# Optimization experiments

Measured on AMD Instinct MI355X. Metric: run time of the kernel, lower is better.

## Reference

```python
import jax, jax.numpy as jnp
import numpy as np

V, E, H, K, B, T = 32000, 512, 1024, 64, 64, 512


def setup_inputs() -> dict:
    key = jax.random.key(0)
    ks = jax.random.split(key, 12)
    nrm = lambda k, shape, sc: jax.random.normal(k, shape, jnp.float32) * sc
    inv_sqrt_h = 1.0 / np.sqrt(H)
    return {
        "x": jax.random.randint(ks[0], (B, T), 0, V),
        "tags": jax.random.randint(ks[1], (B, T), 0, K),
        "emb": nrm(ks[2], (V, E), 0.02),
        "w_ih": nrm(ks[3], (3 * H, E), inv_sqrt_h),
        "w_hh": nrm(ks[4], (3 * H, H), inv_sqrt_h),
        "b_ih": nrm(ks[5], (3 * H,), 0.01),
        "b_hh": nrm(ks[6], (3 * H,), 0.01),
        "fc_w": nrm(ks[7], (K, H), inv_sqrt_h),
        "fc_b": jnp.zeros((K,), jnp.float32),
        "start_trans": nrm(ks[8], (K,), 0.1),
        "end_trans": nrm(ks[9], (K,), 0.1),
        "trans": nrm(ks[10], (K, K), 0.1),
    }


def gru_scan(x_seq, w_ih, w_hh, b_ih, b_hh):
    # x_seq: [T, B, E] -> hidden states [T, B, H]; torch nn.GRU equations.
    Bn = x_seq.shape[1]
    Hd = w_hh.shape[1]
    # precompute input projections for all steps: [T, B, 3H]
    gi = jnp.einsum('tbe,ge->tbg', x_seq, w_ih) + b_ih

    def step(h, gi_t):
        gh = h @ w_hh.T + b_hh                      # [B, 3H]
        i_r, i_z, i_n = jnp.split(gi_t, 3, axis=-1)
        h_r, h_z, h_n = jnp.split(gh, 3, axis=-1)
        r = jax.nn.sigmoid(i_r + h_r)
        z = jax.nn.sigmoid(i_z + h_z)
        n = jnp.tanh(i_n + r * h_n)
        h_new = (1.0 - z) * n + z * h
        return h_new, h_new

    h0 = jnp.zeros((Bn, Hd), x_seq.dtype)
    _, hs = jax.lax.scan(step, h0, gi)
    return hs


def crf_nll(emissions, tags, start, end, trans):
    # emissions [B, T, K], tags [B, T]; torchcrf CRF, mask=None, reduction='sum'.
    em_t = jnp.swapaxes(emissions, 0, 1)   # [T, B, K]
    tg_t = jnp.swapaxes(tags, 0, 1)        # [T, B]
    Bn = emissions.shape[0]
    bidx = jnp.arange(Bn)

    # numerator: score of the gold path
    num0 = start[tg_t[0]] + em_t[0, bidx, tg_t[0]]

    def num_step(acc, xs):
        em_i, tag_prev, tag_cur = xs
        acc = acc + trans[tag_prev, tag_cur] + em_i[bidx, tag_cur]
        return acc, None

    num, _ = jax.lax.scan(num_step, num0, (em_t[1:], tg_t[:-1], tg_t[1:]))
    num = num + end[tg_t[-1]]

    # denominator: forward algorithm (log partition)
    alpha0 = start + em_t[0]                # [B, K]

    def den_step(alpha, em_i):
        # alpha[b,i] + trans[i,j] + em_i[b,j] -> logsumexp over i
        nxt = jax.scipy.special.logsumexp(
            alpha[:, :, None] + trans[None, :, :] + em_i[:, None, :], axis=1)
        return nxt, None

    alpha, _ = jax.lax.scan(den_step, alpha0, em_t[1:])
    den = jax.scipy.special.logsumexp(alpha + end, axis=1)
    return jnp.sum(den - num)  # = -sum(log-likelihood) = model's returned loss


def reference(x, tags, emb, w_ih, w_hh, b_ih, b_hh, fc_w, fc_b,
              start_trans, end_trans, trans):
    xe = emb[x]                              # [B, T, E]
    hs = gru_scan(jnp.swapaxes(xe, 0, 1), w_ih, w_hh, b_ih, b_hh)  # [T, B, H]
    gru_out = jnp.swapaxes(hs, 0, 1)         # [B, T, H]
    emissions = gru_out @ fc_w.T + fc_b      # [B, T, K]
    return crf_nll(emissions, tags, start_trans, end_trans, trans)
```

## Files before the change

### kernel.cpp

```cpp
#include <hip/hip_runtime.h>

typedef unsigned short USH;
typedef unsigned int u32;
typedef unsigned long long u64;
typedef float v4f __attribute__((ext_vector_type(4)));
typedef __bf16 v8bf __attribute__((ext_vector_type(8)));
typedef u32 v4u __attribute__((ext_vector_type(4)));

#define B_ 64
#define T_ 512
#define E_ 512
#define H_ 1024
#define NSCAN 128

__device__ __forceinline__ USH f2b(float x) {
  union { float f; u32 u; } v; v.f = x;
  u32 r = v.u + 0x7FFFu + ((v.u >> 16) & 1u);
  return (USH)(r >> 16);
}
__device__ __forceinline__ v8bf ldb8(const USH* p) {
  uint4 u = *reinterpret_cast<const uint4*>(p);
  return __builtin_bit_cast(v8bf, u);
}
__device__ __forceinline__ v4f MF(v8bf a, v8bf b, v4f c) {
  return __builtin_amdgcn_mfma_f32_16x16x32_bf16(a, b, c, 0, 0, 0);
}
__device__ __forceinline__ float sigm(float x) { return 1.0f / (1.0f + __expf(-x)); }
__device__ __forceinline__ float tanhx(float x) { return 1.0f - 2.0f / (__expf(2.0f * x) + 1.0f); }

__device__ __forceinline__ v4u ldc16(u64 a) {
  v4u d;
  asm volatile("global_load_dwordx4 %0, %1, off sc0 sc1" : "=v"(d) : "v"(a));
  return d;
}
__device__ __forceinline__ void stc16(u64 a, v4u d) {
  asm volatile("global_store_dwordx4 %0, %1, off sc1" :: "v"(a), "v"(d) : "memory");
}

__global__ void castk(const float* __restrict__ s, USH* __restrict__ d, int n) {
  int i = (blockIdx.x * 256 + threadIdx.x) * 4;
  if (i >= n) return;
  float4 v = *reinterpret_cast<const float4*>(s + i);
  ushort4 q = make_ushort4(f2b(v.x), f2b(v.y), f2b(v.z), f2b(v.w));
  *reinterpret_cast<ushort4*>(d + i) = q;
}

__global__ void gatherk(const int* __restrict__ x, const float* __restrict__ emb, USH* __restrict__ xeb) {
  int r = blockIdx.x;
  int id = x[r];
  const float4* e = reinterpret_cast<const float4*>(emb + (long)id * E_);
  float4 v = e[threadIdx.x];
  ushort4 q = make_ushort4(f2b(v.x), f2b(v.y), f2b(v.z), f2b(v.w));
  *reinterpret_cast<ushort4*>(xeb + (long)r * E_ + threadIdx.x * 4) = q;
}

__global__ __launch_bounds__(256, 1) void fused(
    const USH* __restrict__ xeb, const USH* __restrict__ wihB, const USH* __restrict__ whhB,
    const float* __restrict__ bih, const float* __restrict__ bhh, char* __restrict__ hsC,
    const USH* __restrict__ fcwB, const float* __restrict__ fcb, float* __restrict__ em)
{
  __shared__ float redS[6144];
  __shared__ USH  trpS[512];

  const int tid = threadIdx.x;
  const int wv = tid >> 6, ln = tid & 63;
  const int l16 = ln & 15, lq = ln >> 4;
  const v4f z4 = {0.f, 0.f, 0.f, 0.f};

  if (blockIdx.x < NSCAN) {
    const int bg = blockIdx.x >> 6, cb = blockIdx.x & 63;
    const int b0 = bg * 32, c0 = cb * 16;

    v8bf wihf[4][3], whhf[8][3];
    #pragma unroll
    for (int kt = 0; kt < 4; ++kt)
      #pragma unroll
      for (int g = 0; g < 3; ++g)
        wihf[kt][g] = ldb8(wihB + (size_t)(g * H_ + c0 + l16) * E_ + (wv * 16 + kt * 4 + lq) * 8);
    #pragma unroll
    for (int kt = 0; kt < 8; ++kt)
      #pragma unroll
      for (int g = 0; g < 3; ++g)
        whhf[kt][g] = ldb8(whhB + (size_t)(g * H_ + c0 + l16) * H_ + (wv * 32 + kt * 4 + lq) * 8);

    const int cgl = c0 + l16;
    const float bir = bih[cgl], biz = bih[H_ + cgl], bin = bih[2 * H_ + cgl];
    const float bhr = bhh[cgl], bhz = bhh[H_ + cgl], bhn = bhh[2 * H_ + cgl];

    const USH* a1b = xeb + (size_t)(b0 + l16) * (T_ * E_) + wv * 128 + 8 * lq;
    const u64 hC = (u64)(uintptr_t)hsC + (u64)bg * 65536;
    const int lane_off = (wv * 16 + (lq >> 1)) * 1024 + l16 * 32 + (lq & 1) * 16;
    const u64 probe_off = (u64)((wv * 16 + l16) * 1024 + 1020);

    float hp0 = 0.f, hp1 = 0.f, hp2 = 0.f, hp3 = 0.f;
    v4f* rv = reinterpret_cast<v4f*>(redS);

    uint4 pf[8];
    #pragma unroll
    for (int kt = 0; kt < 4; ++kt) {
      pf[kt * 2]     = *reinterpret_cast<const uint4*>(a1b + kt * 32);
      pf[kt * 2 + 1] = *reinterpret_cast<const uint4*>(a1b + 16 * (T_ * E_) + kt * 32);
    }
    u32 pr = 0;

    for (int t = 0; t < T_; ++t) {
      v4f acc[8];
      #pragma unroll
      for (int i = 0; i < 8; ++i) acc[i] = z4;

      #pragma unroll
      for (int kt = 0; kt < 4; ++kt) {
        v8bf a0 = __builtin_bit_cast(v8bf, pf[kt * 2]);
        v8bf a1f = __builtin_bit_cast(v8bf, pf[kt * 2 + 1]);
        acc[0] = MF(a0, wihf[kt][0], acc[0]); acc[1] = MF(a1f, wihf[kt][0], acc[1]);
        acc[2] = MF(a0, wihf[kt][1], acc[2]); acc[3] = MF(a1f, wihf[kt][1], acc[3]);
        acc[4] = MF(a0, wihf[kt][2], acc[4]); acc[5] = MF(a1f, wihf[kt][2], acc[5]);
      }

      if (t > 0) {
        const u64 hbase = hC + (u64)(t - 1) * 131072;
        while (true) {
          asm volatile("s_waitcnt vmcnt(0)" ::: "memory");
          __builtin_amdgcn_sched_barrier(0);
          if (__ballot(pr != 0xFFFFFFFFu) == ~0ull) break;
          asm volatile("global_load_dword %0, %1, off sc0 sc1" : "=v"(pr) : "v"(hbase + probe_off));
        }
        v4u ha[16];
        while (true) {
          #pragma unroll
          for (int kt = 0; kt < 8; ++kt) {
            ha[kt * 2]     = ldc16(hbase + lane_off + kt * 2048);
            ha[kt * 2 + 1] = ldc16(hbase + lane_off + kt * 2048 + 512);
          }
          asm volatile("s_waitcnt vmcnt(0)" ::: "memory");
          __builtin_amdgcn_sched_barrier(0);
          bool bad = false;
          #pragma unroll
          for (int f = 0; f < 16; ++f) {
            #pragma unroll
            for (int d = 0; d < 4; ++d) bad |= (ha[f][d] == 0xFFFFFFFFu);
          }
          if (__ballot(bad) == 0ull) break;
        }
        #pragma unroll
        for (int kt = 0; kt < 8; ++kt) {
          v8bf a0 = __builtin_bit_cast(v8bf, ha[kt * 2]);
          v8bf a1f = __builtin_bit_cast(v8bf, ha[kt * 2 + 1]);
          acc[0] = MF(a0, whhf[kt][0], acc[0]); acc[1] = MF(a1f, whhf[kt][0], acc[1]);
          acc[2] = MF(a0, whhf[kt][1], acc[2]); acc[3] = MF(a1f, whhf[kt][1], acc[3]);
          acc[6] = MF(a0, whhf[kt][2], acc[6]); acc[7] = MF(a1f, whhf[kt][2], acc[7]);
        }
      }

      if (wv >= 2) {
        #pragma unroll
        for (int f = 0; f < 8; ++f) rv[(wv - 2) * 512 + f * 64 + ln] = acc[f];
      } else if (wv == 0) {
        #pragma unroll
        for (int j = 0; j < 4; ++j) rv[1024 + j * 64 + ln] = acc[2 * j + 1];
      } else {
        #pragma unroll
        for (int j = 0; j < 4; ++j) rv[1280 + j * 64 + ln] = acc[2 * j];
      }
      __syncthreads();

      if (wv < 2) {
        v4f m0, m1, m2, m3;
        if (wv == 0) {
          m0 = acc[0]; m1 = acc[2]; m2 = acc[4]; m3 = acc[6];
          #pragma unroll
          for (int w = 0; w < 2; ++w) {
            m0 += rv[w * 512 + 0 * 64 + ln]; m1 += rv[w * 512 + 2 * 64 + ln];
            m2 += rv[w * 512 + 4 * 64 + ln]; m3 += rv[w * 512 + 6 * 64 + ln];
          }
          m0 += rv[1280 + 0 * 64 + ln]; m1 += rv[1280 + 1 * 64 + ln];
          m2 += rv[1280 + 2 * 64 + ln]; m3 += rv[1280 + 3 * 64 + ln];
        } else {
          m0 = acc[1]; m1 = acc[3]; m2 = acc[5]; m3 = acc[7];
          #pragma unroll
          for (int w = 0; w < 2; ++w) {
            m0 += rv[w * 512 + 1 * 64 + ln]; m1 += rv[w * 512 + 3 * 64 + ln];
            m2 += rv[w * 512 + 5 * 64 + ln]; m3 += rv[w * 512 + 7 * 64 + ln];
          }
          m0 += rv[1024 + 0 * 64 + ln]; m1 += rv[1024 + 1 * 64 + ln];
          m2 += rv[1024 + 2 * 64 + ln]; m3 += rv[1024 + 3 * 64 + ln];
        }
        #pragma unroll
        for (int r4 = 0; r4 < 4; ++r4) {
          float rg = sigm(m0[r4] + bir + bhr);
          float zg = sigm(m1[r4] + biz + bhz);
          float ng = tanhx(m2[r4] + bin + rg * (m3[r4] + bhn));
          float hprev = (r4 == 0 ? hp0 : r4 == 1 ? hp1 : r4 == 2 ? hp2 : hp3);
          float hn = (1.f - zg) * ng + zg * hprev;
          if (r4 == 0) hp0 = hn; else if (r4 == 1) hp1 = hn; else if (r4 == 2) hp2 = hn; else hp3 = hn;
          trpS[(wv * 16 + lq * 4 + r4) * 16 + l16] = f2b(hn);
        }
        if (ln < 32) {
          v4u hv = *reinterpret_cast<const v4u*>(trpS + wv * 256 + ln * 8);
          stc16(hC + (u64)t * 131072 + (u64)cb * 1024 + (u64)(wv * 512) + (u64)ln * 16, hv);
        }
      }

      {
        const u64 hb = hC + (u64)t * 131072;
        asm volatile("global_load_dword %0, %1, off sc0 sc1" : "=v"(pr) : "v"(hb + probe_off));
        const USH* a1n = a1b + (size_t)(t + 1 < T_ ? t + 1 : t) * E_;
        #pragma unroll
        for (int kt = 0; kt < 4; ++kt) {
          pf[kt * 2]     = *reinterpret_cast<const uint4*>(a1n + kt * 32);
          pf[kt * 2 + 1] = *reinterpret_cast<const uint4*>(a1n + 16 * (T_ * E_) + kt * 32);
        }
      }
    }
  } else {
    const int e = blockIdx.x - NSCAN;
    v8bf fcf[8][4];
    #pragma unroll
    for (int kt = 0; kt < 8; ++kt)
      #pragma unroll
      for (int nt = 0; nt < 4; ++nt)
        fcf[kt][nt] = ldb8(fcwB + (size_t)(nt * 16 + l16) * H_ + wv * 256 + kt * 32 + 8 * lq);
    float bias[4];
    #pragma unroll
    for (int nt = 0; nt < 4; ++nt) bias[nt] = fcb[nt * 16 + l16];

    v4f* rvE = reinterpret_cast<v4f*>(redS);
    for (int i = 0; i < 16; ++i) {
      int tile = i * 128 + e, t = tile >> 2, bq = tile & 3;
      const u64 ab = (u64)(uintptr_t)hsC + (u64)t * 131072 + (u64)(bq >> 1) * 65536
                   + (u64)((bq & 1) * 16 + l16) * 32 + (u64)(wv * 16 + (lq >> 1)) * 1024 + (u64)(lq & 1) * 16;
      v4u ha[8];
      while (true) {
        #pragma unroll
        for (int kt = 0; kt < 8; ++kt) ha[kt] = ldc16(ab + kt * 2048);
        asm volatile("s_waitcnt vmcnt(0)" ::: "memory");
        __builtin_amdgcn_sched_barrier(0);
        bool bad = false;
        #pragma unroll
        for (int kt = 0; kt < 8; ++kt) {
          #pragma unroll
          for (int d = 0; d < 4; ++d) bad |= (ha[kt][d] == 0xFFFFFFFFu);
        }
        if (__ballot(bad) == 0ull) break;
        __builtin_amdgcn_s_sleep(32);
      }
      v4f acc[4];
      #pragma unroll
      for (int nt = 0; nt < 4; ++nt) acc[nt] = z4;
      #pragma unroll
      for (int kt = 0; kt < 8; ++kt) {
        v8bf a = __builtin_bit_cast(v8bf, ha[kt]);
        #pragma unroll
        for (int nt = 0; nt < 4; ++nt) acc[nt] = MF(a, fcf[kt][nt], acc[nt]);
      }
      __syncthreads();
      if (wv != 0) {
        #pragma unroll
        for (int nt = 0; nt < 4; ++nt) rvE[(wv - 1) * 256 + nt * 64 + ln] = acc[nt];
      }
      __syncthreads();
      if (wv == 0) {
        #pragma unroll
        for (int nt = 0; nt < 4; ++nt) {
          v4f s = acc[nt];
          #pragma unroll
          for (int w = 0; w < 3; ++w) s += rvE[w * 256 + nt * 64 + ln];
          int k = nt * 16 + l16;
          #pragma unroll
          for (int r = 0; r < 4; ++r) {
            int b = bq * 16 + lq * 4 + r;
            em[((size_t)b * T_ + t) * 64 + k] = s[r] + bias[nt];
          }
        }
      }
    }
  }
}

__global__ __launch_bounds__(64) void crfk(const float* __restrict__ em, const int* __restrict__ tags,
                                           const float* __restrict__ st, const float* __restrict__ en,
                                           const float* __restrict__ tr, float* __restrict__ res) {
  int b = blockIdx.x, j = threadIdx.x;
  __shared__ float trs[4096];
  for (int i = j; i < 4096; i += 64) trs[i] = tr[i];
  __syncthreads();
  const int* tg = tags + b * T_;
  const float* e = em + (long)b * T_ * 64;
  float np = 0.f;
  for (int t = j; t < T_; t += 64) {
    int ct = tg[t];
    np += e[t * 64 + ct];
    if (t > 0) np += trs[tg[t - 1] * 64 + ct];
  }
  #pragma unroll
  for (int o = 32; o; o >>= 1) np += __shfl_xor(np, o, 64);
  float num = np + st[tg[0]] + en[tg[T_ - 1]];
  float alpha = st[j] + e[j];
  for (int t = 1; t < T_; ++t) {
    float vv[64];
    #pragma unroll
    for (int i = 0; i < 64; ++i) vv[i] = __shfl(alpha, i, 64) + trs[i * 64 + j];
    float mc[4];
    #pragma unroll
    for (int c = 0; c < 4; ++c) {
      mc[c] = vv[c * 16];
      #pragma unroll
      for (int ii = 1; ii < 16; ++ii) mc[c] = fmaxf(mc[c], vv[c * 16 + ii]);
    }
    float M = fmaxf(fmaxf(mc[0], mc[1]), fmaxf(mc[2], mc[3]));
    float sc[4] = {0.f, 0.f, 0.f, 0.f};
    #pragma unroll
    for (int c = 0; c < 4; ++c)
      #pragma unroll
      for (int ii = 0; ii < 16; ++ii) sc[c] += __expf(vv[c * 16 + ii] - M);
    alpha = M + __logf((sc[0] + sc[1]) + (sc[2] + sc[3])) + e[t * 64 + j];
  }
  float v = alpha + en[j];
  float mm = v;
  #pragma unroll
  for (int o = 32; o; o >>= 1) mm = fmaxf(mm, __shfl_xor(mm, o, 64));
  float ss = __expf(v - mm);
  #pragma unroll
  for (int o = 32; o; o >>= 1) ss += __shfl_xor(ss, o, 64);
  if (j == 0) res[b] = (mm + __logf(ss)) - num;
}

__global__ void fin(const float* __restrict__ res, float* __restrict__ out) {
  float v = res[threadIdx.x];
  #pragma unroll
  for (int o = 32; o; o >>= 1) v += __shfl_xor(v, o, 64);
  if (threadIdx.x == 0) out[0] = v;
}

extern "C" void kernel_launch(void* const* d_in, const int* in_sizes, int n_in,
                              void* d_out, int out_size, void* d_ws, size_t ws_size,
                              hipStream_t stream) {
  (void)in_sizes; (void)n_in; (void)out_size;
  const int*   x    = (const int*)d_in[0];
  const int*   tags = (const int*)d_in[1];
  const float* emb  = (const float*)d_in[2];
  const float* wih  = (const float*)d_in[3];
  const float* whh  = (const float*)d_in[4];
  const float* bih  = (const float*)d_in[5];
  const float* bhh  = (const float*)d_in[6];
  const float* fcw  = (const float*)d_in[7];
  const float* fcb  = (const float*)d_in[8];
  const float* str  = (const float*)d_in[9];
  const float* enr  = (const float*)d_in[10];
  const float* trn  = (const float*)d_in[11];

  char* ws = (char*)d_ws;
  USH*   xeb  = (USH*)(ws + 0);
  USH*   wihB = (USH*)(ws + 33554432);
  USH*   whhB = (USH*)(ws + 36700160);
  USH*   fcwB = (USH*)(ws + 42991616);
  char*  hsC  = (char*)(ws + 43122688);
  float* em   = (float*)(ws + 110231552);
  float* res  = (float*)(ws + 118620160);
  if (ws_size < 118620416ull) return;

  hipMemsetAsync(hsC, 0xFF, 67108864, stream);

  castk<<<1536, 256, 0, stream>>>(wih, wihB, 3 * H_ * E_);
  castk<<<3072, 256, 0, stream>>>(whh, whhB, 3 * H_ * H_);
  castk<<<64, 256, 0, stream>>>(fcw, fcwB, 64 * H_);
  gatherk<<<B_ * T_, 128, 0, stream>>>(x, emb, xeb);
  fused<<<256, 256, 0, stream>>>(xeb, wihB, whhB, bih, bhh, hsC, fcwB, fcb, em);
  crfk<<<B_, 64, 0, stream>>>(em, tags, str, enr, trn, res);
  fin<<<1, 64, 0, stream>>>(res, (float*)d_out);
}
```

Baseline: 2.685 ms.

## Fuse weight casts, CRF and final reduction into persistent kernel with flag sync

Removes the separate bf16 cast kernels by converting the fp32 weights to bf16 inside the fused kernel as they are loaded into registers. The CRF forward pass and the final sum become extra blocks of the persistent kernel that poll emission and result sentinels, so they overlap with the GRU scan. The scan's cross-block wait now uses per-column-block step-counter flags and speculatively prefetches the next hidden state, falling back to flag polling only when sentinels remain. This cuts launches and the serial CRF tail, but adds more spin-polling traffic and a smaller emission block count.

```diff
diff --git a/kernel.cpp b/kernel.cpp
--- a/kernel.cpp
+++ b/kernel.cpp
@@ -12,15 +12,21 @@
 #define E_ 512
 #define H_ 1024
 #define NSCAN 128
+#define EMIT0 128
+#define NEMIT 111
+#define CRF0  239
+#define FINB  255
 
 __device__ __forceinline__ USH f2b(float x) {
   union { float f; u32 u; } v; v.f = x;
   u32 r = v.u + 0x7FFFu + ((v.u >> 16) & 1u);
   return (USH)(r >> 16);
 }
-__device__ __forceinline__ v8bf ldb8(const USH* p) {
-  uint4 u = *reinterpret_cast<const uint4*>(p);
-  return __builtin_bit_cast(v8bf, u);
+__device__ __forceinline__ v8bf pack8(float4 a, float4 b) {
+  union { USH s[8]; v8bf v; } r;
+  r.s[0] = f2b(a.x); r.s[1] = f2b(a.y); r.s[2] = f2b(a.z); r.s[3] = f2b(a.w);
+  r.s[4] = f2b(b.x); r.s[5] = f2b(b.y); r.s[6] = f2b(b.z); r.s[7] = f2b(b.w);
+  return r.v;
 }
 __device__ __forceinline__ v4f MF(v8bf a, v8bf b, v4f c) {
   return __builtin_amdgcn_mfma_f32_16x16x32_bf16(a, b, c, 0, 0, 0);
@@ -36,13 +42,8 @@
 __device__ __forceinline__ void stc16(u64 a, v4u d) {
   asm volatile("global_store_dwordx4 %0, %1, off sc1" :: "v"(a), "v"(d) : "memory");
 }
-
-__global__ void castk(const float* __restrict__ s, USH* __restrict__ d, int n) {
-  int i = (blockIdx.x * 256 + threadIdx.x) * 4;
-  if (i >= n) return;
-  float4 v = *reinterpret_cast<const float4*>(s + i);
-  ushort4 q = make_ushort4(f2b(v.x), f2b(v.y), f2b(v.z), f2b(v.w));
-  *reinterpret_cast<ushort4*>(d + i) = q;
+__device__ __forceinline__ void stdw(u64 a, u32 v) {
+  asm volatile("global_store_dword %0, %1, off sc1" :: "v"(a), "v"(v) : "memory");
 }
 
 __global__ void gatherk(const int* __restrict__ x, const float* __restrict__ emb, USH* __restrict__ xeb) {
@@ -55,9 +56,12 @@
 }
 
 __global__ __launch_bounds__(256, 1) void fused(
-    const USH* __restrict__ xeb, const USH* __restrict__ wihB, const USH* __restrict__ whhB,
+    const USH* __restrict__ xeb, const float* __restrict__ wih, const float* __restrict__ whh,
     const float* __restrict__ bih, const float* __restrict__ bhh, char* __restrict__ hsC,
-    const USH* __restrict__ fcwB, const float* __restrict__ fcb, float* __restrict__ em)
+    u32* __restrict__ flags, const float* __restrict__ fcw, const float* __restrict__ fcb,
+    float* __restrict__ em, const int* __restrict__ tags, const float* __restrict__ stv,
+    const float* __restrict__ env, const float* __restrict__ trn, float* __restrict__ res,
+    float* __restrict__ outp)
 {
   __shared__ float redS[6144];
   __shared__ USH  trpS[512];
@@ -75,13 +79,19 @@
     #pragma unroll
     for (int kt = 0; kt < 4; ++kt)
       #pragma unroll
-      for (int g = 0; g < 3; ++g)
-        wihf[kt][g] = ldb8(wihB + (size_t)(g * H_ + c0 + l16) * E_ + (wv * 16 + kt * 4 + lq) * 8);
+      for (int g = 0; g < 3; ++g) {
+        const float* wp = wih + (size_t)(g * H_ + c0 + l16) * E_ + (wv * 16 + kt * 4 + lq) * 8;
+        wihf[kt][g] = pack8(*reinterpret_cast<const float4*>(wp),
+                            *reinterpret_cast<const float4*>(wp + 4));
+      }
     #pragma unroll
     for (int kt = 0; kt < 8; ++kt)
       #pragma unroll
-      for (int g = 0; g < 3; ++g)
-        whhf[kt][g] = ldb8(whhB + (size_t)(g * H_ + c0 + l16) * H_ + (wv * 32 + kt * 4 + lq) * 8);
+      for (int g = 0; g < 3; ++g) {
+        const float* wp = whh + (size_t)(g * H_ + c0 + l16) * H_ + (wv * 32 + kt * 4 + lq) * 8;
+        whhf[kt][g] = pack8(*reinterpret_cast<const float4*>(wp),
+                            *reinterpret_cast<const float4*>(wp + 4));
+      }
 
     const int cgl = c0 + l16;
     const float bir = bih[cgl], biz = bih[H_ + cgl], bin = bih[2 * H_ + cgl];
@@ -90,7 +100,8 @@
     const USH* a1b = xeb + (size_t)(b0 + l16) * (T_ * E_) + wv * 128 + 8 * lq;
     const u64 hC = (u64)(uintptr_t)hsC + (u64)bg * 65536;
     const int lane_off = (wv * 16 + (lq >> 1)) * 1024 + l16 * 32 + (lq & 1) * 16;
-    const u64 probe_off = (u64)((wv * 16 + l16) * 1024 + 1020);
+    const u64 flv = (u64)(uintptr_t)(flags + (bg * 64 + wv * 16 + l16));
+    const u64 myfl = (u64)(uintptr_t)(flags + (bg * 64 + cb));
 
     float hp0 = 0.f, hp1 = 0.f, hp2 = 0.f, hp3 = 0.f;
     v4f* rv = reinterpret_cast<v4f*>(redS);
@@ -101,7 +112,8 @@
       pf[kt * 2]     = *reinterpret_cast<const uint4*>(a1b + kt * 32);
       pf[kt * 2 + 1] = *reinterpret_cast<const uint4*>(a1b + 16 * (T_ * E_) + kt * 32);
     }
-    u32 pr = 0;
+    u32 fr = 0;
+    v4u ha[16];
 
     for (int t = 0; t < T_; ++t) {
       v4f acc[8];
@@ -119,28 +131,37 @@
 
       if (t > 0) {
         const u64 hbase = hC + (u64)(t - 1) * 131072;
-        while (true) {
-          asm volatile("s_waitcnt vmcnt(0)" ::: "memory");
-          __builtin_amdgcn_sched_barrier(0);
-          if (__ballot(pr != 0xFFFFFFFFu) == ~0ull) break;
-          asm volatile("global_load_dword %0, %1, off sc0 sc1" : "=v"(pr) : "v"(hbase + probe_off));
-        }
-        v4u ha[16];
-        while (true) {
-          #pragma unroll
-          for (int kt = 0; kt < 8; ++kt) {
-            ha[kt * 2]     = ldc16(hbase + lane_off + kt * 2048);
-            ha[kt * 2 + 1] = ldc16(hbase + lane_off + kt * 2048 + 512);
+        asm volatile("s_waitcnt vmcnt(0)" ::: "memory");
+        __builtin_amdgcn_sched_barrier(0);
+        bool bad = false;
+        #pragma unroll
+        for (int f = 0; f < 16; ++f) {
+          #pragma unroll
+          for (int d = 0; d < 4; ++d) bad |= (ha[f][d] == 0xFFFFFFFFu);
+        }
+        if (__ballot(bad) != 0ull) {
+          while (__ballot(fr >= (u32)t) != ~0ull) {
+            asm volatile("global_load_dword %0, %1, off sc0 sc1" : "=v"(fr) : "v"(flv));
+            asm volatile("s_waitcnt vmcnt(0)" ::: "memory");
+            __builtin_amdgcn_sched_barrier(0);
           }
-          asm volatile("s_waitcnt vmcnt(0)" ::: "memory");
-          __builtin_amdgcn_sched_barrier(0);
-          bool bad = false;
-          #pragma unroll
-          for (int f = 0; f < 16; ++f) {
+          while (true) {
             #pragma unroll
-            for (int d = 0; d < 4; ++d) bad |= (ha[f][d] == 0xFFFFFFFFu);
+            for (int kt = 0; kt < 8; ++kt) {
+              ha[kt * 2]     = ldc16(hbase + lane_off + kt * 2048);
+              ha[kt * 2 + 1] = ldc16(hbase + lane_off + kt * 2048 + 512);
+            }
+            asm volatile("s_waitcnt vmcnt(0)" ::: "memory");
+            __builtin_amdgcn_sched_barrier(0);
+            bad = false;
+            #pragma unroll
+            for (int f = 0; f < 16; ++f) {
+              #pragma unroll
+              for (int d = 0; d < 4; ++d) bad |= (ha[f][d] == 0xFFFFFFFFu);
+            }
+            if (__ballot(bad) == 0ull) break;
+            __builtin_amdgcn_s_sleep(1);
           }
-          if (__ballot(bad) == 0ull) break;
         }
         #pragma unroll
         for (int kt = 0; kt < 8; ++kt) {
@@ -199,11 +220,17 @@
           v4u hv = *reinterpret_cast<const v4u*>(trpS + wv * 256 + ln * 8);
           stc16(hC + (u64)t * 131072 + (u64)cb * 1024 + (u64)(wv * 512) + (u64)ln * 16, hv);
         }
+        if (wv == 1 && ln == 0) stdw(myfl, (u32)(t + 1));
       }
 
       {
         const u64 hb = hC + (u64)t * 131072;
-        asm volatile("global_load_dword %0, %1, off sc0 sc1" : "=v"(pr) : "v"(hb + probe_off));
+        #pragma unroll
+        for (int kt = 0; kt < 8; ++kt) {
+          ha[kt * 2]     = ldc16(hb + lane_off + kt * 2048);
+          ha[kt * 2 + 1] = ldc16(hb + lane_off + kt * 2048 + 512);
+        }
+        asm volatile("global_load_dword %0, %1, off sc0 sc1" : "=v"(fr) : "v"(flv));
         const USH* a1n = a1b + (size_t)(t + 1 < T_ ? t + 1 : t) * E_;
         #pragma unroll
         for (int kt = 0; kt < 4; ++kt) {
@@ -212,34 +239,37 @@
         }
       }
     }
-  } else {
-    const int e = blockIdx.x - NSCAN;
+  } else if (blockIdx.x < CRF0) {
+    const int e = blockIdx.x - EMIT0;
     v8bf fcf[8][4];
     #pragma unroll
     for (int kt = 0; kt < 8; ++kt)
       #pragma unroll
-      for (int nt = 0; nt < 4; ++nt)
-        fcf[kt][nt] = ldb8(fcwB + (size_t)(nt * 16 + l16) * H_ + wv * 256 + kt * 32 + 8 * lq);
+      for (int nt = 0; nt < 4; ++nt) {
+        const float* wp = fcw + (size_t)(nt * 16 + l16) * H_ + wv * 256 + kt * 32 + lq * 8;
+        fcf[kt][nt] = pack8(*reinterpret_cast<const float4*>(wp),
+                            *reinterpret_cast<const float4*>(wp + 4));
+      }
     float bias[4];
     #pragma unroll
     for (int nt = 0; nt < 4; ++nt) bias[nt] = fcb[nt * 16 + l16];
 
     v4f* rvE = reinterpret_cast<v4f*>(redS);
-    for (int i = 0; i < 16; ++i) {
-      int tile = i * 128 + e, t = tile >> 2, bq = tile & 3;
+    for (int tile = e; tile < 2048; tile += NEMIT) {
+      int t = tile >> 2, bq = tile & 3;
       const u64 ab = (u64)(uintptr_t)hsC + (u64)t * 131072 + (u64)(bq >> 1) * 65536
                    + (u64)((bq & 1) * 16 + l16) * 32 + (u64)(wv * 16 + (lq >> 1)) * 1024 + (u64)(lq & 1) * 16;
-      v4u ha[8];
+      v4u ha2[8];
       while (true) {
         #pragma unroll
-        for (int kt = 0; kt < 8; ++kt) ha[kt] = ldc16(ab + kt * 2048);
+        for (int kt = 0; kt < 8; ++kt) ha2[kt] = ldc16(ab + kt * 2048);
         asm volatile("s_waitcnt vmcnt(0)" ::: "memory");
         __builtin_amdgcn_sched_barrier(0);
         bool bad = false;
         #pragma unroll
         for (int kt = 0; kt < 8; ++kt) {
           #pragma unroll
-          for (int d = 0; d < 4; ++d) bad |= (ha[kt][d] == 0xFFFFFFFFu);
+          for (int d = 0; d < 4; ++d) bad |= (ha2[kt][d] == 0xFFFFFFFFu);
         }
         if (__ballot(bad) == 0ull) break;
         __builtin_amdgcn_s_sleep(32);
@@ -249,7 +279,7 @@
       for (int nt = 0; nt < 4; ++nt) acc[nt] = z4;
       #pragma unroll
       for (int kt = 0; kt < 8; ++kt) {
-        v8bf a = __builtin_bit_cast(v8bf, ha[kt]);
+        v8bf a = __builtin_bit_cast(v8bf, ha2[kt]);
         #pragma unroll
         for (int nt = 0; nt < 4; ++nt) acc[nt] = MF(a, fcf[kt][nt], acc[nt]);
       }
@@ -269,67 +299,92 @@
           #pragma unroll
           for (int r = 0; r < 4; ++r) {
             int b = bq * 16 + lq * 4 + r;
-            em[((size_t)b * T_ + t) * 64 + k] = s[r] + bias[nt];
+            float val = s[r] + bias[nt];
+            u32 vb; { union { float f; u32 u; } c; c.f = val; vb = c.u; }
+            u64 ea = (u64)(uintptr_t)em + ((((size_t)b * T_ + t) * 64) + k) * 4;
+            stdw(ea, vb);
           }
         }
       }
     }
+  } else if (blockIdx.x < FINB) {
+    float* trsS = redS;
+    int* tgS = (int*)(redS + 4096);
+    for (int i = tid; i < 4096; i += 256) trsS[i] = trn[i];
+    const int b = (blockIdx.x - CRF0) * 4 + wv;
+    for (int i = ln; i < T_; i += 64) tgS[wv * 512 + i] = tags[b * T_ + i];
+    __syncthreads();
+    const int j = ln;
+    const float stj = stv[j], enj = env[j];
+    const u64 emb0 = (u64)(uintptr_t)em + ((size_t)b * T_) * 256 + (size_t)j * 4;
+    float alpha = 0.f, num = 0.f; int tprev = 0;
+    for (int t = 0; t < T_; ++t) {
+      u32 ev;
+      const u64 ea = emb0 + (size_t)t * 256;
+      while (true) {
+        asm volatile("global_load_dword %0, %1, off sc0 sc1" : "=v"(ev) : "v"(ea));
+        asm volatile("s_waitcnt vmcnt(0)" ::: "memory");
+        __builtin_amdgcn_sched_barrier(0);
+        if (__ballot(ev == 0xFFFFFFFFu) == 0ull) break;
+        __builtin_amdgcn_s_sleep(16);
+      }
+      float e; { union { u32 u; float f; } c; c.u = ev; e = c.f; }
+      int ct = tgS[wv * 512 + t];
+      float esh = __shfl(e, ct, 64);
+      if (t == 0) {
+        alpha = stj + e;
+        num = stv[ct] + esh;
+      } else {
+        num += trsS[tprev * 64 + ct] + esh;
+        float vv[64];
+        #pragma unroll
+        for (int i = 0; i < 64; ++i) vv[i] = __shfl(alpha, i, 64) + trsS[i * 64 + j];
+        float mc[4];
+        #pragma unroll
+        for (int c4 = 0; c4 < 4; ++c4) {
+          mc[c4] = vv[c4 * 16];
+          #pragma unroll
+          for (int ii = 1; ii < 16; ++ii) mc[c4] = fmaxf(mc[c4], vv[c4 * 16 + ii]);
+        }
+        float M = fmaxf(fmaxf(mc[0], mc[1]), fmaxf(mc[2], mc[3]));
+        float sc[4] = {0.f, 0.f, 0.f, 0.f};
+        #pragma unroll
+        for (int c4 = 0; c4 < 4; ++c4)
+          #pragma unroll
+          for (int ii = 0; ii < 16; ++ii) sc[c4] += __expf(vv[c4 * 16 + ii] - M);
+        alpha = M + __logf((sc[0] + sc[1]) + (sc[2] + sc[3])) + e;
+      }
+      tprev = ct;
+    }
+    float v = alpha + enj;
+    float mm = v;
+    #pragma unroll
+    for (int o = 32; o; o >>= 1) mm = fmaxf(mm, __shfl_xor(mm, o, 64));
+    float ss = __expf(v - mm);
+    #pragma unroll
+    for (int o = 32; o; o >>= 1) ss += __shfl_xor(ss, o, 64);
+    if (j == 0) {
+      float r = (mm + __logf(ss)) - num;
+      u32 rb; { union { float f; u32 u; } c; c.f = r; rb = c.u; }
+      stdw((u64)(uintptr_t)res + (size_t)b * 4, rb);
+    }
+  } else {
+    if (tid < 64) {
+      u32 rb;
+      const u64 ra = (u64)(uintptr_t)res + (size_t)tid * 4;
+      while (true) {
+        asm volatile("global_load_dword %0, %1, off sc0 sc1" : "=v"(rb) : "v"(ra));
+        asm volatile("s_waitcnt vmcnt(0)" ::: "memory");
+        __builtin_amdgcn_sched_barrier(0);
+        if (__ballot(rb == 0xFFFFFFFFu) == 0ull) break;
+        __builtin_amdgcn_s_sleep(32);
+      }
+      float v; { union { u32 u; float f; } c; c.u = rb; v = c.f; }
+      #pragma unroll
+      for (int o = 32; o; o >>= 1) v += __shfl_xor(v, o, 64);
+      if (tid == 0) outp[0] = v;
+    }
   }
-}
-
-__global__ __launch_bounds__(64) void crfk(const float* __restrict__ em, const int* __restrict__ tags,
-                                           const float* __restrict__ st, const float* __restrict__ en,
-                                           const float* __restrict__ tr, float* __restrict__ res) {
-  int b = blockIdx.x, j = threadIdx.x;
-  __shared__ float trs[4096];
-  for (int i = j; i < 4096; i += 64) trs[i] = tr[i];
-  __syncthreads();
-  const int* tg = tags + b * T_;
-  const float* e = em + (long)b * T_ * 64;
-  float np = 0.f;
-  for (int t = j; t < T_; t += 64) {
-    int ct = tg[t];
-    np += e[t * 64 + ct];
-    if (t > 0) np += trs[tg[t - 1] * 64 + ct];
-  }
-  #pragma unroll
-  for (int o = 32; o; o >>= 1) np += __shfl_xor(np, o, 64);
-  float num = np + st[tg[0]] + en[tg[T_ - 1]];
-  float alpha = st[j] + e[j];
-  for (int t = 1; t < T_; ++t) {
-    float vv[64];
-    #pragma unroll
-    for (int i = 0; i < 64; ++i) vv[i] = __shfl(alpha, i, 64) + trs[i * 64 + j];
-    float mc[4];
-    #pragma unroll
-    for (int c = 0; c < 4; ++c) {
-      mc[c] = vv[c * 16];
-      #pragma unroll
-      for (int ii = 1; ii < 16; ++ii) mc[c] = fmaxf(mc[c], vv[c * 16 + ii]);
-    }
-    float M = fmaxf(fmaxf(mc[0], mc[1]), fmaxf(mc[2], mc[3]));
-    float sc[4] = {0.f, 0.f, 0.f, 0.f};
-    #pragma unroll
-    for (int c = 0; c < 4; ++c)
-      #pragma unroll
-      for (int ii = 0; ii < 16; ++ii) sc[c] += __expf(vv[c * 16 + ii] - M);
-    alpha = M + __logf((sc[0] + sc[1]) + (sc[2] + sc[3])) + e[t * 64 + j];
-  }
-  float v = alpha + en[j];
-  float mm = v;
-  #pragma unroll
-  for (int o = 32; o; o >>= 1) mm = fmaxf(mm, __shfl_xor(mm, o, 64));
-  float ss = __expf(v - mm);
-  #pragma unroll
-  for (int o = 32; o; o >>= 1) ss += __shfl_xor(ss, o, 64);
-  if (j == 0) res[b] = (mm + __logf(ss)) - num;
-}
-
-__global__ void fin(const float* __restrict__ res, float* __restrict__ out) {
-  float v = res[threadIdx.x];
-  #pragma unroll
-  for (int o = 32; o; o >>= 1) v += __shfl_xor(v, o, 64);
-  if (threadIdx.x == 0) out[0] = v;
 }
 
 extern "C" void kernel_launch(void* const* d_in, const int* in_sizes, int n_in,
@@ -350,22 +405,17 @@
   const float* trn  = (const float*)d_in[11];
 
   char* ws = (char*)d_ws;
-  USH*   xeb  = (USH*)(ws + 0);
-  USH*   wihB = (USH*)(ws + 33554432);
-  USH*   whhB = (USH*)(ws + 36700160);
-  USH*   fcwB = (USH*)(ws + 42991616);
-  char*  hsC  = (char*)(ws + 43122688);
-  float* em   = (float*)(ws + 110231552);
-  float* res  = (float*)(ws + 118620160);
-  if (ws_size < 118620416ull) return;
-
-  hipMemsetAsync(hsC, 0xFF, 67108864, stream);
-
-  castk<<<1536, 256, 0, stream>>>(wih, wihB, 3 * H_ * E_);
-  castk<<<3072, 256, 0, stream>>>(whh, whhB, 3 * H_ * H_);
-  castk<<<64, 256, 0, stream>>>(fcw, fcwB, 64 * H_);
+  char*  hsC  = ws;
+  float* em   = (float*)(ws + 67108864);
+  float* res  = (float*)(ws + 75497472);
+  u32*   flags= (u32*)(ws + 75497728);
+  USH*   xeb  = (USH*)(ws + 75499520);
+  if (ws_size < 109053952ull) return;
+
+  hipMemsetAsync(ws, 0xFF, 75497728ull, stream);
+  hipMemsetAsync(ws + 75497728, 0, 512, stream);
+
   gatherk<<<B_ * T_, 128, 0, stream>>>(x, emb, xeb);
-  fused<<<256, 256, 0, stream>>>(xeb, wihB, whhB, bih, bhh, hsC, fcwB, fcb, em);
-  crfk<<<B_, 64, 0, stream>>>(em, tags, str, enr, trn, res);
-  fin<<<1, 64, 0, stream>>>(res, (float*)d_out);
-}
+  fused<<<256, 256, 0, stream>>>(xeb, wih, whh, bih, bhh, hsC, flags, fcw, fcb,
+                                 em, tags, str, enr, trn, res, (float*)d_out);
+}
```

Result: slower. 2.912 ms (+8.4%).
